# Kernel optimization log

Measured on AMD Instinct MI355X. Metric: run time of the kernel, lower is better.

The kernel has to match this reference:

```python
import jax, jax.numpy as jnp
import numpy as np


def setup_inputs() -> dict:
    key = jax.random.key(0)
    k1, k2, k3, k4 = jax.random.split(key, 4)
    N, IN, OUT, R, B = 8192, 256, 256, 8, 4
    a = jax.random.normal(k1, (N, N), dtype=jnp.float32)
    x = jax.random.normal(k2, (N, IN, R), dtype=jnp.float32)
    w_bases = jax.random.normal(k3, (B, IN, OUT), dtype=jnp.float32) * (1.0 / np.sqrt(IN))
    w_rel = jax.random.normal(k4, (R, B), dtype=jnp.float32) * 0.5
    return {"a": a, "x": x, "w_bases": w_bases, "w_rel": w_rel}


def reference(a, x, w_bases, w_rel):
    # Basis-combined per-relation weights: [R, IN, OUT]
    w = jnp.einsum('rb,bio->rio', w_rel, w_bases)
    # Per-relation aggregation: support_r = a @ x[:, :, r] -> stack as [N, R, IN]
    # (matches torch.cat([a @ x[:,:,r] for r], dim=1) ordering)
    supports = jnp.einsum('nm,mir->nri', a, x)  # [N, R, IN]
    # tmp [N, R*IN] @ weights [R*IN, OUT] fused as one einsum
    out = jnp.einsum('nri,rio->no', supports, w)  # [N, OUT]
    return out
```

## Files before the change

kernel.cpp:

```cpp
#include <hip/hip_runtime.h>
#include <hip/hip_bf16.h>

typedef __fp16 f16x2 __attribute__((ext_vector_type(2)));
typedef __fp16 f16x8 __attribute__((ext_vector_type(8)));
typedef float  f32x4 __attribute__((ext_vector_type(4)));

#define NN   8192
#define INC  256
#define OUTC 256
#define RR   8
#define BB   4
#define K2   2048

__global__ void build_w2t(const float* __restrict__ wb, const float* __restrict__ wr,
                          float* __restrict__ W2T) {
    int k = blockIdx.x;
    int o = threadIdx.x;
    int i = k >> 3, r = k & 7;
    float s = 0.f;
#pragma unroll
    for (int b = 0; b < BB; ++b)
        s = fmaf(wr[r * BB + b], wb[((b << 8) + i) * OUTC + o], s);
    W2T[o * K2 + k] = s;
}

constexpr int BM = 128, BN = 128, BK = 32, BKP = 40;

__global__ __launch_bounds__(256, 2)
void gemm_f16_splitk(const float* __restrict__ A, const float* __restrict__ Bt,
                     float* __restrict__ C, int M, int N, int K, int kPerSplit) {
    __shared__ __align__(16) __fp16 As[BM][BKP];
    __shared__ __align__(16) __fp16 Bs[BN][BKP];

    const int bm = blockIdx.x * BM;
    const int bn = blockIdx.y * BN;
    const int k0 = blockIdx.z * kPerSplit;
    const int kEnd = k0 + kPerSplit;

    const int tid  = threadIdx.x;
    const int lane = tid & 63;
    const int wave = tid >> 6;
    const int wm   = (wave >> 1) * 64;
    const int wn   = (wave & 1) * 64;
    const int quad = lane >> 4;
    const int l16  = lane & 15;

    f32x4 acc[4][4];
#pragma unroll
    for (int ti = 0; ti < 4; ++ti)
#pragma unroll
        for (int tj = 0; tj < 4; ++tj)
            acc[ti][tj] = (f32x4){0.f, 0.f, 0.f, 0.f};

    for (int kc = k0; kc < kEnd; kc += BK) {
#pragma unroll
        for (int s = 0; s < 4; ++s) {
            int c   = tid + s * 256;
            int row = c >> 3;
            int kq  = c & 7;
            const float4 v = *reinterpret_cast<const float4*>(
                &A[(size_t)(bm + row) * K + kc + kq * 4]);
            *reinterpret_cast<f16x2*>(&As[row][kq * 4 + 0]) = __builtin_amdgcn_cvt_pkrtz(v.x, v.y);
            *reinterpret_cast<f16x2*>(&As[row][kq * 4 + 2]) = __builtin_amdgcn_cvt_pkrtz(v.z, v.w);
        }
#pragma unroll
        for (int s = 0; s < 4; ++s) {
            int c   = tid + s * 256;
            int row = c >> 3;
            int kq  = c & 7;
            const float4 v = *reinterpret_cast<const float4*>(
                &Bt[(size_t)(bn + row) * K + kc + kq * 4]);
            *reinterpret_cast<f16x2*>(&Bs[row][kq * 4 + 0]) = __builtin_amdgcn_cvt_pkrtz(v.x, v.y);
            *reinterpret_cast<f16x2*>(&Bs[row][kq * 4 + 2]) = __builtin_amdgcn_cvt_pkrtz(v.z, v.w);
        }
        __syncthreads();

        f16x8 af[4], bf[4];
#pragma unroll
        for (int t = 0; t < 4; ++t) {
            af[t] = *reinterpret_cast<const f16x8*>(&As[wm + t * 16 + l16][quad * 8]);
            bf[t] = *reinterpret_cast<const f16x8*>(&Bs[wn + t * 16 + l16][quad * 8]);
        }
#pragma unroll
        for (int ti = 0; ti < 4; ++ti)
#pragma unroll
            for (int tj = 0; tj < 4; ++tj)
                acc[ti][tj] = __builtin_amdgcn_mfma_f32_16x16x32_f16(
                    af[ti], bf[tj], acc[ti][tj], 0, 0, 0);
        __syncthreads();
    }

#pragma unroll
    for (int ti = 0; ti < 4; ++ti) {
#pragma unroll
        for (int tj = 0; tj < 4; ++tj) {
#pragma unroll
            for (int r = 0; r < 4; ++r) {
                int row = bm + wm + ti * 16 + quad * 4 + r;
                int col = bn + wn + tj * 16 + l16;
                atomicAdd(&C[(size_t)row * N + col], acc[ti][tj][r]);
            }
        }
    }
}

extern "C" void kernel_launch(void* const* d_in, const int* in_sizes, int n_in,
                              void* d_out, int out_size, void* d_ws, size_t ws_size,
                              hipStream_t stream) {
    const float* a  = (const float*)d_in[0];
    const float* x  = (const float*)d_in[1];
    const float* wb = (const float*)d_in[2];
    const float* wr = (const float*)d_in[3];
    float* out = (float*)d_out;

    float* W2T = (float*)d_ws;
    float* yT  = (float*)((char*)d_ws + (size_t)OUTC * K2 * 4);

    (void)hipMemsetAsync(yT,  0, (size_t)OUTC * NN * sizeof(float), stream);
    (void)hipMemsetAsync(out, 0, (size_t)NN * OUTC * sizeof(float), stream);

    build_w2t<<<dim3(K2), dim3(256), 0, stream>>>(wb, wr, W2T);

    gemm_f16_splitk<<<dim3(2, 64, 4), dim3(256), 0, stream>>>(
        W2T, x, yT, 256, NN, K2, 512);

    gemm_f16_splitk<<<dim3(64, 2, 8), dim3(256), 0, stream>>>(
        a, yT, out, NN, OUTC, NN, 1024);
}
```

Measured before the change: 521.0 us.

## Use async global-to-LDS loads, fp16 intermediates, and partial-buffer split-K reduction

Tiles now go from global memory straight into LDS with global_load_lds, and fp32 operands are converted to fp16 when fragments are read from LDS instead of before staging. W2T and yT are stored as fp16 to halve their traffic. The atomicAdd split-K epilogue and the memsets are replaced by per-split partial buffers plus separate reduce kernels. The price is extra partial-buffer traffic and additional launches, and the unpadded LDS layout may cause bank conflicts.

Result: faster. 497.4 us (-4.5%).

```diff
diff --git a/kernel.cpp b/kernel.cpp
--- a/kernel.cpp
+++ b/kernel.cpp
@@ -1,41 +1,62 @@
 #include <hip/hip_runtime.h>
 #include <hip/hip_bf16.h>
+#include <stdint.h>
 
 typedef __fp16 f16x2 __attribute__((ext_vector_type(2)));
 typedef __fp16 f16x8 __attribute__((ext_vector_type(8)));
 typedef float  f32x4 __attribute__((ext_vector_type(4)));
 
+#define GLOBAL_AS __attribute__((address_space(1)))
+#define LDS_AS    __attribute__((address_space(3)))
+
 #define NN   8192
 #define INC  256
 #define OUTC 256
-#define RR   8
-#define BB   4
 #define K2   2048
-
-__global__ void build_w2t(const float* __restrict__ wb, const float* __restrict__ wr,
-                          float* __restrict__ W2T) {
-    int k = blockIdx.x;
-    int o = threadIdx.x;
-    int i = k >> 3, r = k & 7;
-    float s = 0.f;
-#pragma unroll
-    for (int b = 0; b < BB; ++b)
-        s = fmaf(wr[r * BB + b], wb[((b << 8) + i) * OUTC + o], s);
-    W2T[o * K2 + k] = s;
-}
-
-constexpr int BM = 128, BN = 128, BK = 32, BKP = 40;
-
+#define YTN  ((size_t)OUTC * NN)
+
+__device__ __forceinline__ void async_copy16(const void* g, void* l) {
+    __builtin_amdgcn_global_load_lds((const GLOBAL_AS uint32_t*)g,
+                                     (LDS_AS uint32_t*)l, 16, 0, 0);
+}
+
+__global__ void build_w2t16(const float* __restrict__ wb, const float* __restrict__ wr,
+                            __fp16* __restrict__ W2T16) {
+    int o = blockIdx.x;
+    int i = threadIdx.x;
+    float s[8];
+#pragma unroll
+    for (int r = 0; r < 8; ++r) s[r] = 0.f;
+#pragma unroll
+    for (int b = 0; b < 4; ++b) {
+        float w = wb[((size_t)((b << 8) + i)) * OUTC + o];
+#pragma unroll
+        for (int r = 0; r < 8; ++r) s[r] = fmaf(wr[r * 4 + b], w, s[r]);
+    }
+    f16x8 out;
+    f16x2* p = (f16x2*)&out;
+    p[0] = __builtin_amdgcn_cvt_pkrtz(s[0], s[1]);
+    p[1] = __builtin_amdgcn_cvt_pkrtz(s[2], s[3]);
+    p[2] = __builtin_amdgcn_cvt_pkrtz(s[4], s[5]);
+    p[3] = __builtin_amdgcn_cvt_pkrtz(s[6], s[7]);
+    *reinterpret_cast<f16x8*>(&W2T16[(size_t)o * K2 + i * 8]) = out;
+}
+
+constexpr int BM = 128, BN = 128, BK = 32;
+
+template <bool AF32, bool BF32>
 __global__ __launch_bounds__(256, 2)
-void gemm_f16_splitk(const float* __restrict__ A, const float* __restrict__ Bt,
-                     float* __restrict__ C, int M, int N, int K, int kPerSplit) {
-    __shared__ __align__(16) __fp16 As[BM][BKP];
-    __shared__ __align__(16) __fp16 Bs[BN][BKP];
+void gemm_mixed(const void* __restrict__ Ap, const void* __restrict__ Bp,
+                float* __restrict__ Cp, int M, int N, int K, int kPerSplit) {
+    constexpr int ABYTES = BM * BK * (AF32 ? 4 : 2);
+    constexpr int BBYTES = BN * BK * (BF32 ? 4 : 2);
+    __shared__ __align__(16) char smem[ABYTES + BBYTES];
+    char* As = smem;
+    char* Bs = smem + ABYTES;
 
     const int bm = blockIdx.x * BM;
     const int bn = blockIdx.y * BN;
     const int k0 = blockIdx.z * kPerSplit;
-    const int kEnd = k0 + kPerSplit;
 
     const int tid  = threadIdx.x;
     const int lane = tid & 63;
@@ -52,34 +73,70 @@
         for (int tj = 0; tj < 4; ++tj)
             acc[ti][tj] = (f32x4){0.f, 0.f, 0.f, 0.f};
 
-    for (int kc = k0; kc < kEnd; kc += BK) {
-#pragma unroll
-        for (int s = 0; s < 4; ++s) {
-            int c   = tid + s * 256;
-            int row = c >> 3;
-            int kq  = c & 7;
-            const float4 v = *reinterpret_cast<const float4*>(
-                &A[(size_t)(bm + row) * K + kc + kq * 4]);
-            *reinterpret_cast<f16x2*>(&As[row][kq * 4 + 0]) = __builtin_amdgcn_cvt_pkrtz(v.x, v.y);
-            *reinterpret_cast<f16x2*>(&As[row][kq * 4 + 2]) = __builtin_amdgcn_cvt_pkrtz(v.z, v.w);
+    for (int kc = k0; kc < k0 + kPerSplit; kc += BK) {
+        if (AF32) {
+            const float* Ag = (const float*)Ap;
+#pragma unroll
+            for (int i = 0; i < 4; ++i) {
+                int r0 = wave * 32 + i * 8;
+                const float* g = Ag + (size_t)(bm + r0 + (lane >> 3)) * K + kc + ((lane & 7) << 2);
+                async_copy16(g, As + (size_t)r0 * BK * 4);
+            }
+        } else {
+            const __fp16* Ag = (const __fp16*)Ap;
+#pragma unroll
+            for (int i = 0; i < 2; ++i) {
+                int r0 = wave * 32 + i * 16;
+                const __fp16* g = Ag + (size_t)(bm + r0 + (lane >> 2)) * K + kc + ((lane & 3) << 3);
+                async_copy16(g, As + (size_t)r0 * BK * 2);
+            }
         }
-#pragma unroll
-        for (int s = 0; s < 4; ++s) {
-            int c   = tid + s * 256;
-            int row = c >> 3;
-            int kq  = c & 7;
-            const float4 v = *reinterpret_cast<const float4*>(
-                &Bt[(size_t)(bn + row) * K + kc + kq * 4]);
-            *reinterpret_cast<f16x2*>(&Bs[row][kq * 4 + 0]) = __builtin_amdgcn_cvt_pkrtz(v.x, v.y);
-            *reinterpret_cast<f16x2*>(&Bs[row][kq * 4 + 2]) = __builtin_amdgcn_cvt_pkrtz(v.z, v.w);
+        if (BF32) {
+            const float* Bg = (const float*)Bp;
+#pragma unroll
+            for (int i = 0; i < 4; ++i) {
+                int r0 = wave * 32 + i * 8;
+                const float* g = Bg + (size_t)(bn + r0 + (lane >> 3)) * K + kc + ((lane & 7) << 2);
+                async_copy16(g, Bs + (size_t)r0 * BK * 4);
+            }
+        } else {
+            const __fp16* Bg = (const __fp16*)Bp;
+#pragma unroll
+            for (int i = 0; i < 2; ++i) {
+                int r0 = wave * 32 + i * 16;
+                const __fp16* g = Bg + (size_t)(bn + r0 + (lane >> 2)) * K + kc + ((lane & 3) << 3);
+                async_copy16(g, Bs + (size_t)r0 * BK * 2);
+            }
         }
         __syncthreads();
 
         f16x8 af[4], bf[4];
 #pragma unroll
         for (int t = 0; t < 4; ++t) {
-            af[t] = *reinterpret_cast<const f16x8*>(&As[wm + t * 16 + l16][quad * 8]);
-            bf[t] = *reinterpret_cast<const f16x8*>(&Bs[wn + t * 16 + l16][quad * 8]);
+            if (AF32) {
+                const float* Ar = (const float*)As + (size_t)(wm + t * 16 + l16) * BK + quad * 8;
+                f32x4 u0 = *(const f32x4*)Ar;
+                f32x4 u1 = *(const f32x4*)(Ar + 4);
+                f16x2* p = (f16x2*)&af[t];
+                p[0] = __builtin_amdgcn_cvt_pkrtz(u0[0], u0[1]);
+                p[1] = __builtin_amdgcn_cvt_pkrtz(u0[2], u0[3]);
+                p[2] = __builtin_amdgcn_cvt_pkrtz(u1[0], u1[1]);
+                p[3] = __builtin_amdgcn_cvt_pkrtz(u1[2], u1[3]);
+            } else {
+                af[t] = *(const f16x8*)((const __fp16*)As + (size_t)(wm + t * 16 + l16) * BK + quad * 8);
+            }
+            if (BF32) {
+                const float* Br = (const float*)Bs + (size_t)(wn + t * 16 + l16) * BK + quad * 8;
+                f32x4 u0 = *(const f32x4*)Br;
+                f32x4 u1 = *(const f32x4*)(Br + 4);
+                f16x2* p = (f16x2*)&bf[t];
+                p[0] = __builtin_amdgcn_cvt_pkrtz(u0[0], u0[1]);
+                p[1] = __builtin_amdgcn_cvt_pkrtz(u0[2], u0[3]);
+                p[2] = __builtin_amdgcn_cvt_pkrtz(u1[0], u1[1]);
+                p[3] = __builtin_amdgcn_cvt_pkrtz(u1[2], u1[3]);
+            } else {
+                bf[t] = *(const f16x8*)((const __fp16*)Bs + (size_t)(wn + t * 16 + l16) * BK + quad * 8);
+            }
         }
 #pragma unroll
         for (int ti = 0; ti < 4; ++ti)
@@ -90,18 +147,45 @@
         __syncthreads();
     }
 
-#pragma unroll
-    for (int ti = 0; ti < 4; ++ti) {
-#pragma unroll
-        for (int tj = 0; tj < 4; ++tj) {
+    float* Cz = Cp + (size_t)blockIdx.z * M * N;
+#pragma unroll
+    for (int ti = 0; ti < 4; ++ti)
+#pragma unroll
+        for (int tj = 0; tj < 4; ++tj)
 #pragma unroll
             for (int r = 0; r < 4; ++r) {
                 int row = bm + wm + ti * 16 + quad * 4 + r;
                 int col = bn + wn + tj * 16 + l16;
-                atomicAdd(&C[(size_t)row * N + col], acc[ti][tj][r]);
-            }
-        }
+                Cz[(size_t)row * N + col] = acc[ti][tj][r];
+            }
+}
+
+__global__ void reduce_yT(const float* __restrict__ yTp, __fp16* __restrict__ yT16) {
+    size_t base = ((size_t)blockIdx.x * 256 + threadIdx.x) * 8;
+    f32x4 s0 = (f32x4){0.f, 0.f, 0.f, 0.f};
+    f32x4 s1 = (f32x4){0.f, 0.f, 0.f, 0.f};
+#pragma unroll
+    for (int z = 0; z < 4; ++z) {
+        const float* p = yTp + (size_t)z * YTN + base;
+        s0 += *(const f32x4*)p;
+        s1 += *(const f32x4*)(p + 4);
     }
+    f16x8 out;
+    f16x2* p = (f16x2*)&out;
+    p[0] = __builtin_amdgcn_cvt_pkrtz(s0[0], s0[1]);
+    p[1] = __builtin_amdgcn_cvt_pkrtz(s0[2], s0[3]);
+    p[2] = __builtin_amdgcn_cvt_pkrtz(s1[0], s1[1]);
+    p[3] = __builtin_amdgcn_cvt_pkrtz(s1[2], s1[3]);
+    *reinterpret_cast<f16x8*>(&yT16[base]) = out;
+}
+
+__global__ void reduce_out(const float* __restrict__ op, float* __restrict__ out) {
+    size_t base = ((size_t)blockIdx.x * 256 + threadIdx.x) * 4;
+    f32x4 s = (f32x4){0.f, 0.f, 0.f, 0.f};
+#pragma unroll
+    for (int z = 0; z < 8; ++z)
+        s += *(const f32x4*)(op + (size_t)z * YTN + base);
+    *reinterpret_cast<f32x4*>(&out[base]) = s;
 }
 
 extern "C" void kernel_launch(void* const* d_in, const int* in_sizes, int n_in,
@@ -113,17 +197,21 @@
     const float* wr = (const float*)d_in[3];
     float* out = (float*)d_out;
 
-    float* W2T = (float*)d_ws;
-    float* yT  = (float*)((char*)d_ws + (size_t)OUTC * K2 * 4);
-
-    (void)hipMemsetAsync(yT,  0, (size_t)OUTC * NN * sizeof(float), stream);
-    (void)hipMemsetAsync(out, 0, (size_t)NN * OUTC * sizeof(float), stream);
-
-    build_w2t<<<dim3(K2), dim3(256), 0, stream>>>(wb, wr, W2T);
-
-    gemm_f16_splitk<<<dim3(2, 64, 4), dim3(256), 0, stream>>>(
-        W2T, x, yT, 256, NN, K2, 512);
-
-    gemm_f16_splitk<<<dim3(64, 2, 8), dim3(256), 0, stream>>>(
-        a, yT, out, NN, OUTC, NN, 1024);
-}
+    char* w = (char*)d_ws;
+    float*  yT_p  = (float*)(w);
+    __fp16* yT16  = (__fp16*)(w + ((size_t)32 << 20));
+    float*  out_p = (float*)(w + ((size_t)36 << 20));
+    __fp16* W2T16 = (__fp16*)(w + ((size_t)100 << 20));
+
+    build_w2t16<<<dim3(256), dim3(256), 0, stream>>>(wb, wr, W2T16);
+
+    gemm_mixed<false, true><<<dim3(2, 64, 4), dim3(256), 0, stream>>>(
+        W2T16, x, yT_p, 256, NN, K2, 512);
+
+    reduce_yT<<<dim3(1024), dim3(256), 0, stream>>>(yT_p, yT16);
+
+    gemm_mixed<true, false><<<dim3(64, 2, 8), dim3(256), 0, stream>>>(
+        a, yT16, out_p, NN, OUTC, NN, 1024);
+
+    reduce_out<<<dim3(2048), dim3(256), 0, stream>>>(out_p, out);
+}
```
